# Kernel optimization log

Hardware: AMD Instinct MI355X
Metric: run time of the kernel (lower is better)

The kernel has to match this reference:

```python
import jax, jax.numpy as jnp
import numpy as np

STAGE_NUM = 3
BN_EPS = 1e-5

def _l2norm(t, axis):
    return t / (1e-6 + jnp.linalg.norm(t, axis=axis, keepdims=True))

def setup_inputs() -> dict:
    key = jax.random.key(0)
    ks = jax.random.split(key, 5)
    b, c, h, w, k = 16, 512, 64, 64, 64
    x = jax.random.normal(ks[0], (b, c, h, w), jnp.float32)
    mu = jax.random.normal(ks[1], (1, c, k), jnp.float32) * np.sqrt(2.0 / k)
    mu = _l2norm(mu, axis=1)
    conv1_w = jax.random.normal(ks[2], (c, c), jnp.float32) * np.sqrt(2.0 / c)
    conv1_b = jnp.zeros((c,), jnp.float32)
    conv2_w = jax.random.normal(ks[3], (c, c), jnp.float32) * np.sqrt(2.0 / c)
    bn_gamma = jnp.ones((c,), jnp.float32)
    bn_beta = jnp.zeros((c,), jnp.float32)
    return {"x": x, "mu": mu, "conv1_w": conv1_w, "conv1_b": conv1_b,
            "conv2_w": conv2_w, "bn_gamma": bn_gamma, "bn_beta": bn_beta}

def reference(x, mu, conv1_w, conv1_b, conv2_w, bn_gamma, bn_beta):
    b, c, h, w = x.shape
    idn = x
    # conv1: 1x1 conv == per-pixel matmul
    xf = jnp.einsum('oc,bchw->bohw', conv1_w, x) + conv1_b[None, :, None, None]
    xf = xf.reshape(b, c, h * w)            # [b,c,n]
    mu_b = jnp.broadcast_to(mu, (b, c, mu.shape[2]))  # [b,c,k]
    z = None
    for _ in range(STAGE_NUM):
        z = jax.nn.softmax(jnp.einsum('bcn,bck->bnk', xf, mu_b), axis=2)  # [b,n,k]
        z_ = z / (1e-6 + jnp.sum(z, axis=1, keepdims=True))
        mu_b = _l2norm(jnp.einsum('bcn,bnk->bck', xf, z_), axis=1)
    # torch.no_grad(): mu and z are constants w.r.t. autodiff
    mu_b = jax.lax.stop_gradient(mu_b)
    z = jax.lax.stop_gradient(z)
    recon = jnp.einsum('bck,bnk->bcn', mu_b, z).reshape(b, c, h, w)
    recon = jax.nn.relu(recon)
    # conv2 (1x1, no bias) + BatchNorm2d (training: batch stats, biased var)
    y = jnp.einsum('oc,bchw->bohw', conv2_w, recon)
    mean = jnp.mean(y, axis=(0, 2, 3), keepdims=True)
    var = jnp.var(y, axis=(0, 2, 3), keepdims=True)
    y = (y - mean) * jax.lax.rsqrt(var + BN_EPS)
    y = y * bn_gamma[None, :, None, None] + bn_beta[None, :, None, None]
    return jax.nn.relu(y + idn)
```

## Files before the change

kernel.cpp:

```cpp
#include <hip/hip_runtime.h>
#include <math.h>

#define CDIM 512
#define NDIM 4096
#define KDIM 64
#define BDIM 16
#define NSPLIT 8

typedef __attribute__((ext_vector_type(8))) _Float16 f16x8;
typedef __attribute__((ext_vector_type(4))) _Float16 f16x4;
typedef __attribute__((ext_vector_type(4))) float f32x4;

__device__ __forceinline__ void g2lds16(const void* g, void* l) {
  __builtin_amdgcn_global_load_lds(
      (const __attribute__((address_space(1))) int*)g,
      (__attribute__((address_space(3))) int*)l, 16, 0, 0);
}

__device__ __forceinline__ f16x8 ldsfrag(const short* base, int row, int kk,
                                         int lh) {
  int slot = (kk * 4 + lh) ^ (row & 7);
  return *reinterpret_cast<const f16x8*>(&base[row * 64 + slot * 8]);
}

__global__ __launch_bounds__(256) void k_cvtT16(const float* __restrict__ in,
                                                _Float16* __restrict__ outT) {
  __shared__ __align__(16) _Float16 T[64][80];
  const int t = threadIdx.x;
  const int n0 = blockIdx.x * 64, c0 = blockIdx.y * 64;
  const float* ib = in + (size_t)blockIdx.z * CDIM * NDIM;
  _Float16* ob = outT + (size_t)blockIdx.z * NDIM * CDIM;
#pragma unroll
  for (int i = 0; i < 4; ++i) {
    int idx = i * 256 + t;
    int cl = idx >> 4, f4 = idx & 15;
    float4 v = *reinterpret_cast<const float4*>(
        &ib[(size_t)(c0 + cl) * NDIM + n0 + f4 * 4]);
    T[f4 * 4 + 0][cl] = (_Float16)v.x;
    T[f4 * 4 + 1][cl] = (_Float16)v.y;
    T[f4 * 4 + 2][cl] = (_Float16)v.z;
    T[f4 * 4 + 3][cl] = (_Float16)v.w;
  }
  __syncthreads();
#pragma unroll
  for (int i = 0; i < 2; ++i) {
    int idx = i * 256 + t;
    int nl = idx >> 3, ch = idx & 7;
    uint4 u = *reinterpret_cast<const uint4*>(&T[nl][ch * 8]);
    *reinterpret_cast<uint4*>(&ob[(size_t)(n0 + nl) * CDIM + c0 + ch * 8]) = u;
  }
}

__global__ void k_cvt_w16(const float* __restrict__ w,
                          _Float16* __restrict__ wh) {
  int i = (blockIdx.x * 256 + threadIdx.x) * 4;
  float4 v = *reinterpret_cast<const float4*>(&w[i]);
  wh[i] = (_Float16)v.x; wh[i + 1] = (_Float16)v.y;
  wh[i + 2] = (_Float16)v.z; wh[i + 3] = (_Float16)v.w;
}

__global__ __launch_bounds__(256) void k_conv1_16(
    const _Float16* __restrict__ xT, const _Float16* __restrict__ w1,
    const float* __restrict__ b1, _Float16* __restrict__ xfT,
    _Float16* __restrict__ xf) {
  __shared__ __align__(16) short smem[17408];
  short* At = smem;
  short* Bt = smem + 8192;
  const int tid = threadIdx.x;
  const int l = tid & 63, w = tid >> 6;
  const int wm = w >> 1, wn = w & 1;
  const int lr = l & 15, lh = l >> 4;
  const int i0 = blockIdx.x * 128;
  const int j0 = blockIdx.y * 128;
  const int b = blockIdx.z;
  const short* Ag = (const short*)(xT + (size_t)b * NDIM * CDIM);
  const short* Bg = (const short*)w1;
  f32x4 acc[4][4] = {};
  for (int c0 = 0; c0 < CDIM; c0 += 64) {
#pragma unroll
    for (int i = 0; i < 4; ++i) {
      int slot = i * 256 + tid;
      int r = slot >> 3, s = slot & 7, sp = s ^ (r & 7);
      g2lds16(Ag + (size_t)(i0 + r) * CDIM + c0 + sp * 8, At + slot * 8);
    }
#pragma unroll
    for (int i = 0; i < 4; ++i) {
      int slot = i * 256 + tid;
      int r = slot >> 3, s = slot & 7, sp = s ^ (r & 7);
      g2lds16(Bg + (size_t)(j0 + r) * CDIM + c0 + sp * 8, Bt + slot * 8);
    }
    __syncthreads();
#pragma unroll
    for (int kk = 0; kk < 2; ++kk) {
      f16x8 af[4], bf[4];
#pragma unroll
      for (int m = 0; m < 4; ++m) af[m] = ldsfrag(At, wm * 64 + m * 16 + lr, kk, lh);
#pragma unroll
      for (int nf = 0; nf < 4; ++nf) bf[nf] = ldsfrag(Bt, wn * 64 + nf * 16 + lr, kk, lh);
#pragma unroll
      for (int m = 0; m < 4; ++m)
#pragma unroll
        for (int nf = 0; nf < 4; ++nf)
          acc[m][nf] = __builtin_amdgcn_mfma_f32_16x16x32_f16(af[m], bf[nf],
                                                              acc[m][nf], 0, 0, 0);
    }
    __syncthreads();
  }
  _Float16* Otf = (_Float16*)smem;
  _Float16* ob = xfT + (size_t)b * NDIM * CDIM;
#pragma unroll
  for (int m = 0; m < 4; ++m) {
#pragma unroll
    for (int nf = 0; nf < 4; ++nf) {
      int ol = wn * 64 + nf * 16 + lr;
      float bv = b1[j0 + ol];
#pragma unroll
      for (int r = 0; r < 4; ++r) {
        int nl = wm * 64 + m * 16 + lh * 4 + r;
        _Float16 hv = (_Float16)(acc[m][nf][r] + bv);
        ob[(size_t)(i0 + nl) * CDIM + j0 + ol] = hv;
        Otf[ol * 136 + nl] = hv;
      }
    }
  }
  __syncthreads();
  _Float16* xfb = xf + (size_t)b * CDIM * NDIM;
#pragma unroll
  for (int i = 0; i < 8; ++i) {
    int seg = i * 256 + tid;
    int row = seg >> 4, cs = seg & 15;
    f16x8 v = *reinterpret_cast<const f16x8*>(&Otf[row * 136 + cs * 8]);
    *reinterpret_cast<f16x8*>(&xfb[(size_t)(j0 + row) * NDIM + i0 + cs * 8]) = v;
  }
}

__global__ __launch_bounds__(256) void k_conv2_16(
    const _Float16* __restrict__ w2, const _Float16* __restrict__ reconT,
    _Float16* __restrict__ y16, float* __restrict__ bnsum,
    float* __restrict__ bnsumsq) {
  __shared__ __align__(16) short At[128 * 64];
  __shared__ __align__(16) short Bt[128 * 64];
  __shared__ float bns[128], bnq[128];
  const int tid = threadIdx.x;
  const int l = tid & 63, w = tid >> 6;
  const int wm = w >> 1, wn = w & 1;
  const int lr = l & 15, lh = l >> 4;
  const int i0 = blockIdx.x * 128;
  const int j0 = blockIdx.y * 128;
  const int b = blockIdx.z;
  if (tid < 128) { bns[tid] = 0.f; bnq[tid] = 0.f; }
  const short* Ag = (const short*)w2;
  const short* Bg = (const short*)(reconT + (size_t)b * NDIM * CDIM);
  f32x4 acc[4][4] = {};
  for (int c0 = 0; c0 < CDIM; c0 += 64) {
#pragma unroll
    for (int i = 0; i < 4; ++i) {
      int slot = i * 256 + tid;
      int r = slot >> 3, s = slot & 7, sp = s ^ (r & 7);
      g2lds16(Ag + (size_t)(i0 + r) * CDIM + c0 + sp * 8, At + slot * 8);
    }
#pragma unroll
    for (int i = 0; i < 4; ++i) {
      int slot = i * 256 + tid;
      int r = slot >> 3, s = slot & 7, sp = s ^ (r & 7);
      g2lds16(Bg + (size_t)(j0 + r) * CDIM + c0 + sp * 8, Bt + slot * 8);
    }
    __syncthreads();
#pragma unroll
    for (int kk = 0; kk < 2; ++kk) {
      f16x8 af[4], bf[4];
#pragma unroll
      for (int m = 0; m < 4; ++m) af[m] = ldsfrag(At, wm * 64 + m * 16 + lr, kk, lh);
#pragma unroll
      for (int nf = 0; nf < 4; ++nf) bf[nf] = ldsfrag(Bt, wn * 64 + nf * 16 + lr, kk, lh);
#pragma unroll
      for (int m = 0; m < 4; ++m)
#pragma unroll
        for (int nf = 0; nf < 4; ++nf)
          acc[m][nf] = __builtin_amdgcn_mfma_f32_16x16x32_f16(af[m], bf[nf],
                                                              acc[m][nf], 0, 0, 0);
    }
    __syncthreads();
  }
  _Float16* yb = y16 + (size_t)b * CDIM * NDIM;
#pragma unroll
  for (int m = 0; m < 4; ++m) {
#pragma unroll
    for (int r = 0; r < 4; ++r) {
      int ol = wm * 64 + m * 16 + lh * 4 + r;
      float ps = 0.f, pq = 0.f;
#pragma unroll
      for (int nf = 0; nf < 4; ++nf) {
        float v = acc[m][nf][r];
        ps += v; pq += v * v;
        yb[(size_t)(i0 + ol) * NDIM + j0 + wn * 64 + nf * 16 + lr] = (_Float16)v;
      }
#pragma unroll
      for (int d = 1; d < 16; d <<= 1) {
        ps += __shfl_xor(ps, d);
        pq += __shfl_xor(pq, d);
      }
      if (lr == 0) { atomicAdd(&bns[ol], ps); atomicAdd(&bnq[ol], pq); }
    }
  }
  __syncthreads();
  if (tid < 128) {
    atomicAdd(&bnsum[i0 + tid], bns[tid]);
    atomicAdd(&bnsumsq[i0 + tid], bnq[tid]);
  }
}

__global__ void k_init_mu16(const float* __restrict__ mu,
                            _Float16* __restrict__ muT) {
  int idx = blockIdx.x * 256 + threadIdx.x;
  int rem = idx & 32767;
  int k = rem >> 9, c = rem & 511;
  muT[idx] = (_Float16)mu[c * KDIM + k];
}

__global__ __launch_bounds__(256) void k_s1_16(const _Float16* __restrict__ xfT,
                                               const _Float16* __restrict__ muT,
                                               _Float16* __restrict__ z,
                                               _Float16* __restrict__ zT,
                                               float* __restrict__ colsum) {
  __shared__ __align__(16) short At[64 * 64];
  __shared__ __align__(16) short Bt[64 * 64];
  __shared__ __align__(16) _Float16 zs[64][72];
  const int tid = threadIdx.x;
  const int l = tid & 63, w = tid >> 6;
  const int lr = l & 15, lh = l >> 4;
  const int n0 = blockIdx.x * 64;
  const int b = blockIdx.y;
  const short* Ag = (const short*)(xfT + (size_t)b * NDIM * CDIM);
  const short* Bg = (const short*)(muT + (size_t)b * KDIM * CDIM);
  f32x4 acc[4] = {};
  for (int c0 = 0; c0 < CDIM; c0 += 64) {
#pragma unroll
    for (int i = 0; i < 2; ++i) {
      int slot = i * 256 + tid;
      int r = slot >> 3, s = slot & 7, sp = s ^ (r & 7);
      g2lds16(Ag + (size_t)(n0 + r) * CDIM + c0 + sp * 8, At + slot * 8);
    }
#pragma unroll
    for (int i = 0; i < 2; ++i) {
      int slot = i * 256 + tid;
      int r = slot >> 3, s = slot & 7, sp = s ^ (r & 7);
      g2lds16(Bg + (size_t)r * CDIM + c0 + sp * 8, Bt + slot * 8);
    }
    __syncthreads();
#pragma unroll
    for (int kk = 0; kk < 2; ++kk) {
      f16x8 af = ldsfrag(At, w * 16 + lr, kk, lh);
#pragma unroll
      for (int kf = 0; kf < 4; ++kf) {
        f16x8 bf = ldsfrag(Bt, kf * 16 + lr, kk, lh);
        acc[kf] = __builtin_amdgcn_mfma_f32_16x16x32_f16(af, bf, acc[kf], 0, 0, 0);
      }
    }
    __syncthreads();
  }
#pragma unroll
  for (int r = 0; r < 4; ++r) {
    float m = fmaxf(fmaxf(acc[0][r], acc[1][r]), fmaxf(acc[2][r], acc[3][r]));
#pragma unroll
    for (int d = 8; d >= 1; d >>= 1) m = fmaxf(m, __shfl_xor(m, d));
    float e[4], s = 0.f;
#pragma unroll
    for (int kf = 0; kf < 4; ++kf) { e[kf] = __expf(acc[kf][r] - m); s += e[kf]; }
#pragma unroll
    for (int d = 8; d >= 1; d >>= 1) s += __shfl_xor(s, d);
    float inv = 1.f / s;
    int row = w * 16 + lh * 4 + r;
#pragma unroll
    for (int kf = 0; kf < 4; ++kf) zs[row][kf * 16 + lr] = (_Float16)(e[kf] * inv);
  }
  __syncthreads();
  _Float16* zb = z + (size_t)b * NDIM * KDIM;
  _Float16* zTb = zT + (size_t)b * KDIM * NDIM;
#pragma unroll
  for (int i = 0; i < 2; ++i) {
    int idx = i * 256 + tid;
    int n = idx >> 3, ch = idx & 7;
    *reinterpret_cast<uint4*>(&zb[(size_t)(n0 + n) * KDIM + ch * 8]) =
        *reinterpret_cast<const uint4*>(&zs[n][ch * 8]);
  }
#pragma unroll
  for (int i = 0; i < 2; ++i) {
    int idx = i * 256 + tid;
    int k = idx >> 3, nch = idx & 7;
    f16x8 v;
#pragma unroll
    for (int j = 0; j < 8; ++j) v[j] = zs[nch * 8 + j][k];
    *reinterpret_cast<f16x8*>(&zTb[(size_t)k * NDIM + n0 + nch * 8]) = v;
  }
  if (tid < 64) {
    float s = 0.f;
#pragma unroll
    for (int n = 0; n < 64; ++n) s += (float)zs[n][tid];
    atomicAdd(&colsum[b * KDIM + tid], s);
  }
}

__global__ __launch_bounds__(256) void k_s2_16(const _Float16* __restrict__ zT,
                                               const _Float16* __restrict__ xf,
                                               float* __restrict__ mupart) {
  __shared__ __align__(16) short At[64 * 64];
  __shared__ __align__(16) short Bt[64 * 64];
  const int tid = threadIdx.x;
  const int l = tid & 63, w = tid >> 6;
  const int lr = l & 15, lh = l >> 4;
  const int c0 = blockIdx.x * 64;
  const int split = blockIdx.y;
  const int b = blockIdx.z;
  const short* Ag = (const short*)(zT + (size_t)b * KDIM * NDIM);
  const short* Bg = (const short*)(xf + (size_t)b * CDIM * NDIM);
  f32x4 acc[4] = {};
  for (int st = 0; st < 8; ++st) {
    const int nb = split * (NDIM / NSPLIT) + st * 64;
#pragma unroll
    for (int i = 0; i < 2; ++i) {
      int slot = i * 256 + tid;
      int r = slot >> 3, s = slot & 7, sp = s ^ (r & 7);
      g2lds16(Ag + (size_t)r * NDIM + nb + sp * 8, At + slot * 8);
    }
#pragma unroll
    for (int i = 0; i < 2; ++i) {
      int slot = i * 256 + tid;
      int r = slot >> 3, s = slot & 7, sp = s ^ (r & 7);
      g2lds16(Bg + (size_t)(c0 + r) * NDIM + nb + sp * 8, Bt + slot * 8);
    }
    __syncthreads();
#pragma unroll
    for (int kk = 0; kk < 2; ++kk) {
      f16x8 bf = ldsfrag(Bt, w * 16 + lr, kk, lh);
#pragma unroll
      for (int kf = 0; kf < 4; ++kf) {
        f16x8 af = ldsfrag(At, kf * 16 + lr, kk, lh);
        acc[kf] = __builtin_amdgcn_mfma_f32_16x16x32_f16(af, bf, acc[kf], 0, 0, 0);
      }
    }
    __syncthreads();
  }
  float* mp = mupart + ((size_t)(split * BDIM + b) * KDIM) * CDIM;
#pragma unroll
  for (int kf = 0; kf < 4; ++kf) {
    int k = kf * 16 + lh * 4;
#pragma unroll
    for (int r = 0; r < 4; ++r)
      mp[(size_t)(k + r) * CDIM + c0 + w * 16 + lr] = acc[kf][r];
  }
}

__global__ __launch_bounds__(256) void k_s2red(const float* __restrict__ mupart,
                                               const float* __restrict__ colsum,
                                               _Float16* __restrict__ muT,
                                               _Float16* __restrict__ mu_ck) {
  __shared__ float red[4];
  const int tid = threadIdx.x;
  const int b = blockIdx.x >> 6, k = blockIdx.x & 63;
  float v0 = 0.f, v1 = 0.f;
#pragma unroll
  for (int s = 0; s < NSPLIT; ++s) {
    const float* mp = mupart + ((size_t)(s * BDIM + b) * KDIM + k) * CDIM;
    v0 += mp[tid];
    v1 += mp[tid + 256];
  }
  float ssq = v0 * v0 + v1 * v1;
#pragma unroll
  for (int d = 32; d >= 1; d >>= 1) ssq += __shfl_down(ssq, d);
  if ((tid & 63) == 0) red[tid >> 6] = ssq;
  __syncthreads();
  float tot = red[0] + red[1] + red[2] + red[3];
  float scs = 1.f / (1e-6f + colsum[b * KDIM + k]);
  float inv = scs / (1e-6f + scs * sqrtf(tot));
  _Float16 o0 = (_Float16)(v0 * inv), o1 = (_Float16)(v1 * inv);
  muT[((size_t)b * KDIM + k) * CDIM + tid] = o0;
  muT[((size_t)b * KDIM + k) * CDIM + tid + 256] = o1;
  mu_ck[((size_t)b * CDIM + tid) * KDIM + k] = o0;
  mu_ck[((size_t)b * CDIM + tid + 256) * KDIM + k] = o1;
}

__global__ __launch_bounds__(256) void k_recon16(const _Float16* __restrict__ z,
                                                 const _Float16* __restrict__ mu_ck,
                                                 _Float16* __restrict__ reconT) {
  __shared__ __align__(16) short Az[128 * 64];
  __shared__ __align__(16) short Bm[128 * 64];
  const int tid = threadIdx.x;
  const int l = tid & 63, w = tid >> 6;
  const int wm = w >> 1, wn = w & 1;
  const int lr = l & 15, lh = l >> 4;
  const int n0 = blockIdx.x * 128;
  const int c0 = blockIdx.y * 128;
  const int b = blockIdx.z;
  const short* Ag = (const short*)(z + (size_t)b * NDIM * KDIM);
  const short* Bg = (const short*)(mu_ck + (size_t)b * CDIM * KDIM);
#pragma unroll
  for (int i = 0; i < 4; ++i) {
    int slot = i * 256 + tid;
    int r = slot >> 3, s = slot & 7, sp = s ^ (r & 7);
    g2lds16(Ag + (size_t)(n0 + r) * KDIM + sp * 8, Az + slot * 8);
  }
#pragma unroll
  for (int i = 0; i < 4; ++i) {
    int slot = i * 256 + tid;
    int r = slot >> 3, s = slot & 7, sp = s ^ (r & 7);
    g2lds16(Bg + (size_t)(c0 + r) * KDIM + sp * 8, Bm + slot * 8);
  }
  __syncthreads();
  f32x4 acc[4][4] = {};
#pragma unroll
  for (int kk = 0; kk < 2; ++kk) {
    f16x8 af[4], bf[4];
#pragma unroll
    for (int m = 0; m < 4; ++m) af[m] = ldsfrag(Az, wm * 64 + m * 16 + lr, kk, lh);
#pragma unroll
    for (int nf = 0; nf < 4; ++nf) bf[nf] = ldsfrag(Bm, wn * 64 + nf * 16 + lr, kk, lh);
#pragma unroll
    for (int m = 0; m < 4; ++m)
#pragma unroll
      for (int nf = 0; nf < 4; ++nf)
        acc[m][nf] = __builtin_amdgcn_mfma_f32_16x16x32_f16(af[m], bf[nf],
                                                            acc[m][nf], 0, 0, 0);
  }
  _Float16* ob = reconT + (size_t)b * NDIM * CDIM;
#pragma unroll
  for (int m = 0; m < 4; ++m) {
#pragma unroll
    for (int r = 0; r < 4; ++r) {
      int n = n0 + wm * 64 + m * 16 + lh * 4 + r;
#pragma unroll
      for (int nf = 0; nf < 4; ++nf) {
        int c = c0 + wn * 64 + nf * 16 + lr;
        ob[(size_t)n * CDIM + c] = (_Float16)fmaxf(acc[m][nf][r], 0.f);
      }
    }
  }
}

__global__ void k_final(float* __restrict__ out, const _Float16* __restrict__ y16,
                        const float* __restrict__ x,
                        const float* __restrict__ bnsum,
                        const float* __restrict__ bnsumsq,
                        const float* __restrict__ gamma,
                        const float* __restrict__ beta) {
  const float invM = 1.f / (BDIM * (float)NDIM);
  const size_t total4 = (size_t)BDIM * CDIM * NDIM / 4;
  for (size_t i4 = (size_t)blockIdx.x * 256 + threadIdx.x; i4 < total4;
       i4 += (size_t)gridDim.x * 256) {
    int c = (int)((i4 >> 10) & (CDIM - 1));
    float mean = bnsum[c] * invM;
    float var = bnsumsq[c] * invM - mean * mean;
    float sc = rsqrtf(var + 1e-5f) * gamma[c];
    float sh = beta[c] - mean * sc;
    f16x4 yv = *reinterpret_cast<const f16x4*>(&y16[i4 * 4]);
    float4 xv = reinterpret_cast<const float4*>(x)[i4];
    float4 o;
    o.x = fmaxf(fmaf((float)yv[0], sc, sh) + xv.x, 0.f);
    o.y = fmaxf(fmaf((float)yv[1], sc, sh) + xv.y, 0.f);
    o.z = fmaxf(fmaf((float)yv[2], sc, sh) + xv.z, 0.f);
    o.w = fmaxf(fmaf((float)yv[3], sc, sh) + xv.w, 0.f);
    reinterpret_cast<float4*>(out)[i4] = o;
  }
}

extern "C" void kernel_launch(void* const* d_in, const int* in_sizes, int n_in,
                              void* d_out, int out_size, void* d_ws,
                              size_t ws_size, hipStream_t stream) {
  const float* x = (const float*)d_in[0];
  const float* mu = (const float*)d_in[1];
  const float* w1 = (const float*)d_in[2];
  const float* b1 = (const float*)d_in[3];
  const float* w2 = (const float*)d_in[4];
  const float* gamma = (const float*)d_in[5];
  const float* beta = (const float*)d_in[6];
  float* out = (float*)d_out;

  _Float16* xfT = (_Float16*)d_out;
  _Float16* xf = (_Float16*)d_out + 33554432;

  _Float16* wsH = (_Float16*)d_ws;
  _Float16* xT = wsH;
  _Float16* reconT = wsH;
  _Float16* z = wsH + 33554432;
  _Float16* zT = z + 4194304;
  _Float16* muT = zT + 4194304;
  _Float16* mu_ck = muT + 524288;
  _Float16* w1h = mu_ck + 524288;
  _Float16* w2h = w1h + 262144;
  float* wsF = (float*)(w2h + 262144);
  float* mupart = wsF;
  float* colsum = mupart + 4194304;
  float* bnsum = colsum + 1024;
  float* bnsumsq = bnsum + 512;
  _Float16* y16 = (_Float16*)(bnsumsq + 512);

  k_cvtT16<<<dim3(NDIM / 64, CDIM / 64, BDIM), 256, 0, stream>>>(x, xT);
  k_cvt_w16<<<CDIM * CDIM / 1024, 256, 0, stream>>>(w1, w1h);
  k_cvt_w16<<<CDIM * CDIM / 1024, 256, 0, stream>>>(w2, w2h);

  k_conv1_16<<<dim3(NDIM / 128, CDIM / 128, BDIM), 256, 0, stream>>>(
      xT, w1h, b1, xfT, xf);
  k_init_mu16<<<2048, 256, 0, stream>>>(mu, muT);

  for (int s = 0; s < 3; ++s) {
    hipMemsetAsync(colsum, 0, 1024 * sizeof(float), stream);
    k_s1_16<<<dim3(NDIM / 64, BDIM), 256, 0, stream>>>(xfT, muT, z, zT, colsum);
    k_s2_16<<<dim3(CDIM / 64, NSPLIT, BDIM), 256, 0, stream>>>(zT, xf, mupart);
    k_s2red<<<KDIM * BDIM, 256, 0, stream>>>(mupart, colsum, muT, mu_ck);
  }

  k_recon16<<<dim3(NDIM / 128, CDIM / 128, BDIM), 256, 0, stream>>>(z, mu_ck,
                                                                    reconT);
  hipMemsetAsync(bnsum, 0, 1024 * sizeof(float), stream);
  k_conv2_16<<<dim3(CDIM / 128, NDIM / 128, BDIM), 256, 0, stream>>>(
      w2h, reconT, y16, bnsum, bnsumsq);

  k_final<<<4096, 256, 0, stream>>>(out, y16, x, bnsum, bnsumsq, gamma, beta);
}
```

Measured before the change: 396.6 us.

## Enlarge EM-stage GEMM tiles to 128 rows and swap conv2 grid order

```diff
diff --git a/kernel.cpp b/kernel.cpp
--- a/kernel.cpp
+++ b/kernel.cpp
@@ -145,8 +145,8 @@
   const int l = tid & 63, w = tid >> 6;
   const int wm = w >> 1, wn = w & 1;
   const int lr = l & 15, lh = l >> 4;
-  const int i0 = blockIdx.x * 128;
-  const int j0 = blockIdx.y * 128;
+  const int i0 = blockIdx.y * 128;
+  const int j0 = blockIdx.x * 128;
   const int b = blockIdx.z;
   if (tid < 128) { bns[tid] = 0.f; bnq[tid] = 0.f; }
   const short* Ag = (const short*)w2;
@@ -223,98 +223,115 @@
                                                _Float16* __restrict__ z,
                                                _Float16* __restrict__ zT,
                                                float* __restrict__ colsum) {
-  __shared__ __align__(16) short At[64 * 64];
+  __shared__ __align__(16) short At[128 * 64];
   __shared__ __align__(16) short Bt[64 * 64];
-  __shared__ __align__(16) _Float16 zs[64][72];
+  __shared__ __align__(16) _Float16 zs[128][72];
+  __shared__ float csum[4][64];
   const int tid = threadIdx.x;
   const int l = tid & 63, w = tid >> 6;
   const int lr = l & 15, lh = l >> 4;
-  const int n0 = blockIdx.x * 64;
+  const int n0 = blockIdx.x * 128;
   const int b = blockIdx.y;
   const short* Ag = (const short*)(xfT + (size_t)b * NDIM * CDIM);
   const short* Bg = (const short*)(muT + (size_t)b * KDIM * CDIM);
-  f32x4 acc[4] = {};
+  f32x4 acc[2][4] = {};
   for (int c0 = 0; c0 < CDIM; c0 += 64) {
 #pragma unroll
+    for (int i = 0; i < 4; ++i) {
+      int slot = i * 256 + tid;
+      int r = slot >> 3, s = slot & 7, sp = s ^ (r & 7);
+      g2lds16(Ag + (size_t)(n0 + r) * CDIM + c0 + sp * 8, At + slot * 8);
+    }
+#pragma unroll
     for (int i = 0; i < 2; ++i) {
       int slot = i * 256 + tid;
       int r = slot >> 3, s = slot & 7, sp = s ^ (r & 7);
-      g2lds16(Ag + (size_t)(n0 + r) * CDIM + c0 + sp * 8, At + slot * 8);
-    }
-#pragma unroll
-    for (int i = 0; i < 2; ++i) {
-      int slot = i * 256 + tid;
-      int r = slot >> 3, s = slot & 7, sp = s ^ (r & 7);
       g2lds16(Bg + (size_t)r * CDIM + c0 + sp * 8, Bt + slot * 8);
     }
     __syncthreads();
 #pragma unroll
     for (int kk = 0; kk < 2; ++kk) {
-      f16x8 af = ldsfrag(At, w * 16 + lr, kk, lh);
+      f16x8 af[2], bf;
+#pragma unroll
+      for (int nf = 0; nf < 2; ++nf)
+        af[nf] = ldsfrag(At, w * 32 + nf * 16 + lr, kk, lh);
 #pragma unroll
       for (int kf = 0; kf < 4; ++kf) {
-        f16x8 bf = ldsfrag(Bt, kf * 16 + lr, kk, lh);
-        acc[kf] = __builtin_amdgcn_mfma_f32_16x16x32_f16(af, bf, acc[kf], 0, 0, 0);
+        bf = ldsfrag(Bt, kf * 16 + lr, kk, lh);
+#pragma unroll
+        for (int nf = 0; nf < 2; ++nf)
+          acc[nf][kf] = __builtin_amdgcn_mfma_f32_16x16x32_f16(af[nf], bf,
+                                                               acc[nf][kf], 0, 0, 0);
       }
     }
     __syncthreads();
   }
 #pragma unroll
-  for (int r = 0; r < 4; ++r) {
-    float m = fmaxf(fmaxf(acc[0][r], acc[1][r]), fmaxf(acc[2][r], acc[3][r]));
-#pragma unroll
-    for (int d = 8; d >= 1; d >>= 1) m = fmaxf(m, __shfl_xor(m, d));
-    float e[4], s = 0.f;
-#pragma unroll
-    for (int kf = 0; kf < 4; ++kf) { e[kf] = __expf(acc[kf][r] - m); s += e[kf]; }
-#pragma unroll
-    for (int d = 8; d >= 1; d >>= 1) s += __shfl_xor(s, d);
-    float inv = 1.f / s;
-    int row = w * 16 + lh * 4 + r;
-#pragma unroll
-    for (int kf = 0; kf < 4; ++kf) zs[row][kf * 16 + lr] = (_Float16)(e[kf] * inv);
+  for (int nf = 0; nf < 2; ++nf) {
+#pragma unroll
+    for (int r = 0; r < 4; ++r) {
+      float m = fmaxf(fmaxf(acc[nf][0][r], acc[nf][1][r]),
+                      fmaxf(acc[nf][2][r], acc[nf][3][r]));
+#pragma unroll
+      for (int d = 8; d >= 1; d >>= 1) m = fmaxf(m, __shfl_xor(m, d));
+      float e[4], s = 0.f;
+#pragma unroll
+      for (int kf = 0; kf < 4; ++kf) { e[kf] = __expf(acc[nf][kf][r] - m); s += e[kf]; }
+#pragma unroll
+      for (int d = 8; d >= 1; d >>= 1) s += __shfl_xor(s, d);
+      float inv = 1.f / s;
+      int row = w * 32 + nf * 16 + lh * 4 + r;
+#pragma unroll
+      for (int kf = 0; kf < 4; ++kf)
+        zs[row][kf * 16 + lr] = (_Float16)(e[kf] * inv);
+    }
   }
   __syncthreads();
   _Float16* zb = z + (size_t)b * NDIM * KDIM;
   _Float16* zTb = zT + (size_t)b * KDIM * NDIM;
 #pragma unroll
-  for (int i = 0; i < 2; ++i) {
+  for (int i = 0; i < 4; ++i) {
     int idx = i * 256 + tid;
     int n = idx >> 3, ch = idx & 7;
     *reinterpret_cast<uint4*>(&zb[(size_t)(n0 + n) * KDIM + ch * 8]) =
         *reinterpret_cast<const uint4*>(&zs[n][ch * 8]);
   }
 #pragma unroll
-  for (int i = 0; i < 2; ++i) {
+  for (int i = 0; i < 4; ++i) {
     int idx = i * 256 + tid;
-    int k = idx >> 3, nch = idx & 7;
+    int k = idx >> 4, nch = idx & 15;
     f16x8 v;
 #pragma unroll
     for (int j = 0; j < 8; ++j) v[j] = zs[nch * 8 + j][k];
     *reinterpret_cast<f16x8*>(&zTb[(size_t)k * NDIM + n0 + nch * 8]) = v;
   }
-  if (tid < 64) {
+  {
+    int k = tid & 63, q = tid >> 6;
     float s = 0.f;
 #pragma unroll
-    for (int n = 0; n < 64; ++n) s += (float)zs[n][tid];
-    atomicAdd(&colsum[b * KDIM + tid], s);
-  }
+    for (int n = 0; n < 32; ++n) s += (float)zs[q * 32 + n][k];
+    csum[q][k] = s;
+  }
+  __syncthreads();
+  if (tid < 64)
+    atomicAdd(&colsum[b * KDIM + tid],
+              csum[0][tid] + csum[1][tid] + csum[2][tid] + csum[3][tid]);
 }
 
 __global__ __launch_bounds__(256) void k_s2_16(const _Float16* __restrict__ zT,
                                                const _Float16* __restrict__ xf,
                                                float* __restrict__ mupart) {
   __shared__ __align__(16) short At[64 * 64];
-  __shared__ __align__(16) short Bt[64 * 64];
+  __shared__ __align__(16) short Bt[128 * 64];
   const int tid = threadIdx.x;
   const int l = tid & 63, w = tid >> 6;
   const int lr = l & 15, lh = l >> 4;
-  const int c0 = blockIdx.x * 64;
+  const int c0 = blockIdx.x * 128;
   const int split = blockIdx.y;
   const int b = blockIdx.z;
   const short* Ag = (const short*)(zT + (size_t)b * KDIM * NDIM);
   const short* Bg = (const short*)(xf + (size_t)b * CDIM * NDIM);
-  f32x4 acc[4] = {};
+  f32x4 acc[4][2] = {};
   for (int st = 0; st < 8; ++st) {
     const int nb = split * (NDIM / NSPLIT) + st * 64;
 #pragma unroll
@@ -324,7 +341,7 @@
       g2lds16(Ag + (size_t)r * NDIM + nb + sp * 8, At + slot * 8);
     }
 #pragma unroll
-    for (int i = 0; i < 2; ++i) {
+    for (int i = 0; i < 4; ++i) {
       int slot = i * 256 + tid;
       int r = slot >> 3, s = slot & 7, sp = s ^ (r & 7);
       g2lds16(Bg + (size_t)(c0 + r) * NDIM + nb + sp * 8, Bt + slot * 8);
@@ -332,11 +349,17 @@
     __syncthreads();
 #pragma unroll
     for (int kk = 0; kk < 2; ++kk) {
-      f16x8 bf = ldsfrag(Bt, w * 16 + lr, kk, lh);
+      f16x8 bf[2], af;
+#pragma unroll
+      for (int cf = 0; cf < 2; ++cf)
+        bf[cf] = ldsfrag(Bt, w * 32 + cf * 16 + lr, kk, lh);
 #pragma unroll
       for (int kf = 0; kf < 4; ++kf) {
-        f16x8 af = ldsfrag(At, kf * 16 + lr, kk, lh);
-        acc[kf] = __builtin_amdgcn_mfma_f32_16x16x32_f16(af, bf, acc[kf], 0, 0, 0);
+        af = ldsfrag(At, kf * 16 + lr, kk, lh);
+#pragma unroll
+        for (int cf = 0; cf < 2; ++cf)
+          acc[kf][cf] = __builtin_amdgcn_mfma_f32_16x16x32_f16(af, bf[cf],
+                                                               acc[kf][cf], 0, 0, 0);
       }
     }
     __syncthreads();
@@ -347,7 +370,9 @@
     int k = kf * 16 + lh * 4;
 #pragma unroll
     for (int r = 0; r < 4; ++r)
-      mp[(size_t)(k + r) * CDIM + c0 + w * 16 + lr] = acc[kf][r];
+#pragma unroll
+      for (int cf = 0; cf < 2; ++cf)
+        mp[(size_t)(k + r) * CDIM + c0 + w * 32 + cf * 16 + lr] = acc[kf][cf][r];
   }
 }
 
@@ -504,15 +529,15 @@
 
   for (int s = 0; s < 3; ++s) {
     hipMemsetAsync(colsum, 0, 1024 * sizeof(float), stream);
-    k_s1_16<<<dim3(NDIM / 64, BDIM), 256, 0, stream>>>(xfT, muT, z, zT, colsum);
-    k_s2_16<<<dim3(CDIM / 64, NSPLIT, BDIM), 256, 0, stream>>>(zT, xf, mupart);
+    k_s1_16<<<dim3(NDIM / 128, BDIM), 256, 0, stream>>>(xfT, muT, z, zT, colsum);
+    k_s2_16<<<dim3(CDIM / 128, NSPLIT, BDIM), 256, 0, stream>>>(zT, xf, mupart);
     k_s2red<<<KDIM * BDIM, 256, 0, stream>>>(mupart, colsum, muT, mu_ck);
   }
 
   k_recon16<<<dim3(NDIM / 128, CDIM / 128, BDIM), 256, 0, stream>>>(z, mu_ck,
                                                                     reconT);
   hipMemsetAsync(bnsum, 0, 1024 * sizeof(float), stream);
-  k_conv2_16<<<dim3(CDIM / 128, NDIM / 128, BDIM), 256, 0, stream>>>(
+  k_conv2_16<<<dim3(NDIM / 128, CDIM / 128, BDIM), 256, 0, stream>>>(
       w2h, reconT, y16, bnsum, bnsumsq);
 
   k_final<<<4096, 256, 0, stream>>>(out, y16, x, bnsum, bnsumsq, gamma, beta);
```

Result: faster. 382.4 us (-3.6%).
